# Kernel tuning notes

Hardware: AMD Instinct MI355X
Metric: run time of the kernel (lower is better)

## Reference

```python
import jax, jax.numpy as jnp
import numpy as np

HEAD_SIZE = 64
N_EMBD = 1024
BLOCK_SIZE = 2048


def setup_inputs() -> dict:
    key = jax.random.key(0)
    kx, kk, kq, kv = jax.random.split(key, 4)
    B, T = 8, 2048
    x = jax.random.normal(kx, (B, T, N_EMBD), dtype=jnp.float32)
    # nnx.Linear kernels have shape (in_features, out_features); lecun-normal-ish scale
    s = 1.0 / np.sqrt(N_EMBD)
    Wk = jax.random.normal(kk, (N_EMBD, HEAD_SIZE), dtype=jnp.float32) * s
    Wq = jax.random.normal(kq, (N_EMBD, HEAD_SIZE), dtype=jnp.float32) * s
    Wv = jax.random.normal(kv, (N_EMBD, HEAD_SIZE), dtype=jnp.float32) * s
    return {"x": x, "Wk": Wk, "Wq": Wq, "Wv": Wv}


def reference(x, Wk, Wq, Wv):
    B, T, C = x.shape
    k = jnp.einsum("btc,ch->bth", x, Wk)  # [B,T,H]
    q = jnp.einsum("btc,ch->bth", x, Wq)
    v = jnp.einsum("btc,ch->bth", x, Wv)
    # NOTE: original scales by C**-0.5 where C = n_embd (not head_size)
    scale = jnp.float32(C) ** -0.5
    wei = jnp.einsum("bth,bsh->bts", q, k) * scale  # [B,T,T]
    causal = jnp.tril(jnp.ones((T, T), dtype=bool))
    wei = jnp.where(causal, wei, -jnp.inf)
    wei = jax.nn.softmax(wei, axis=-1)
    # dropout_rate = 0.0 -> identity
    out = jnp.einsum("bts,bsh->bth", wei, v)  # [B,T,H]
    return out
```

## Files before the change

### kernel.cpp

```cpp
#include <hip/hip_runtime.h>
#include <hip/hip_bf16.h>

#define TT 2048
#define BATCH 8
#define MROWS (BATCH*TT)
#define AW 8

typedef __attribute__((ext_vector_type(8))) short bf16x8;
typedef __attribute__((ext_vector_type(4))) short s16x4;
typedef __attribute__((ext_vector_type(4))) float f32x4;

__device__ __forceinline__ short f2bf(float f) {
    union { __hip_bfloat16 h; short s; } u;
    u.h = __float2bfloat16(f);
    return u.s;
}
__device__ __forceinline__ float bf2f(short s) {
    union { unsigned u; float f; } u;
    u.u = ((unsigned)(unsigned short)s) << 16;
    return u.f;
}

typedef __attribute__((address_space(3))) unsigned int       lds_u32_t;
typedef const __attribute__((address_space(1))) unsigned int g_u32_t;
__device__ __forceinline__ void gl_lds16(const void* g, void* l) {
    __builtin_amdgcn_global_load_lds((g_u32_t*)g, (lds_u32_t*)l, 16, 0, 0);
}

__global__ __launch_bounds__(256) void wtrans_kernel(
    const float* __restrict__ Wk, const float* __restrict__ Wq,
    const float* __restrict__ Wv, short* __restrict__ wt)
{
    __shared__ float tile[64][68];
    const int mat = blockIdx.x >> 4;
    const int k0  = (blockIdx.x & 15) * 64;
    const float* W = (mat == 0) ? Wq : (mat == 1) ? Wk : Wv;
    const float scl = (mat == 0) ? 0.04508422002778011f : 1.0f;
    const int t = threadIdx.x;
    const int row = t >> 2, quad = t & 3;
    #pragma unroll
    for (int i = 0; i < 4; i++) {
        float4 v = *(const float4*)(W + (size_t)(k0 + row) * 64 + quad * 16 + i * 4);
        *(float4*)&tile[row][quad * 16 + i * 4] = v;
    }
    __syncthreads();
    short tmp[16];
    #pragma unroll
    for (int j = 0; j < 16; j++) tmp[j] = f2bf(tile[quad * 16 + j][row] * scl);
    short* dst = wt + (size_t)(mat * 64 + row) * 1024 + k0 + quad * 16;
    #pragma unroll
    for (int j2 = 0; j2 < 2; j2++) {
        bf16x8 o;
        #pragma unroll
        for (int jj = 0; jj < 8; jj++) o[jj] = tmp[j2 * 8 + jj];
        *(bf16x8*)(dst + j2 * 8) = o;
    }
}

__global__ __launch_bounds__(512, 2) void proj_kernel(
    const float* __restrict__ x, const short* __restrict__ wt,
    short* __restrict__ qb, short* __restrict__ kb, short* __restrict__ vtb)
{
    __shared__ __align__(16) char lds[131072];

    const int tid  = threadIdx.x;
    const int lane = tid & 63, w = tid >> 6;
    const int l15  = lane & 15, g = lane >> 4;
    const int x7   = l15 & 7;
    const int wr   = w & 1;
    const int wc   = w >> 1;
    const int r0   = blockIdx.x * 64;

    const int arow_s = tid >> 3, aseg = tid & 7;
    const float* xsrc = x + (size_t)(r0 + arow_s) * 1024 + aseg * 16;
    const int ac0 = ((aseg * 2)     ^ (arow_s & 7)) * 16;
    const int ac1 = ((aseg * 2 + 1) ^ (arow_s & 7)) * 16;
    char* const arow_lds0 = lds + arow_s * 256;

    const short* bg[6]; unsigned bOff[6];
    #pragma unroll
    for (int j = 0; j < 6; j++) {
        const int jp   = w * 6 + j;
        const int row  = jp * 4 + (lane >> 4);
        const int slot = (lane & 15) ^ (row & 7);
        bg[j]   = wt + (size_t)row * 1024 + slot * 8;
        bOff[j] = 32768 + jp * 1024;
    }

    f32x4 acc[2][3];
    #pragma unroll
    for (int rt = 0; rt < 2; rt++)
        #pragma unroll
        for (int nt = 0; nt < 3; nt++) acc[rt][nt] = (f32x4){0.f, 0.f, 0.f, 0.f};

    {
        float4 a0 = *(const float4*)(xsrc);
        float4 a1 = *(const float4*)(xsrc + 4);
        float4 a2 = *(const float4*)(xsrc + 8);
        float4 a3 = *(const float4*)(xsrc + 12);
        #pragma unroll
        for (int j = 0; j < 6; j++) gl_lds16(bg[j], lds + bOff[j]);
        bf16x8 c0 = { f2bf(a0.x), f2bf(a0.y), f2bf(a0.z), f2bf(a0.w),
                      f2bf(a1.x), f2bf(a1.y), f2bf(a1.z), f2bf(a1.w) };
        bf16x8 c1 = { f2bf(a2.x), f2bf(a2.y), f2bf(a2.z), f2bf(a2.w),
                      f2bf(a3.x), f2bf(a3.y), f2bf(a3.z), f2bf(a3.w) };
        *(bf16x8*)(arow_lds0 + ac0) = c0;
        *(bf16x8*)(arow_lds0 + ac1) = c1;
    }
    __syncthreads();

    #pragma unroll
    for (int ks = 0; ks < 8; ks++) {
        const int cur = ks & 1;
        const int nb  = cur ^ 1;

        float4 a0, a1, a2, a3;
        if (ks < 7) {
            a0 = *(const float4*)(xsrc + (ks + 1) * 128);
            a1 = *(const float4*)(xsrc + (ks + 1) * 128 + 4);
            a2 = *(const float4*)(xsrc + (ks + 1) * 128 + 8);
            a3 = *(const float4*)(xsrc + (ks + 1) * 128 + 12);
            #pragma unroll
            for (int j = 0; j < 6; j++)
                gl_lds16(bg[j] + (ks + 1) * 128, lds + nb * 49152 + bOff[j]);
        }

        const char*  Ab = lds + cur * 16384;
        const short* Bb = (const short*)(lds + 32768 + cur * 49152);

        bf16x8 af[2][4];
        #pragma unroll
        for (int rt = 0; rt < 2; rt++) {
            const int arow = wr * 32 + rt * 16 + l15;
            #pragma unroll
            for (int kc = 0; kc < 4; kc++)
                af[rt][kc] = *(const bf16x8*)(
                    Ab + arow * 256 + (((kc * 4 + g) ^ x7) * 16));
        }
        bf16x8 bfr[3][4];
        #pragma unroll
        for (int nt = 0; nt < 3; nt++)
            #pragma unroll
            for (int kc = 0; kc < 4; kc++)
                bfr[nt][kc] = *(const bf16x8*)(
                    Bb + (wc * 48 + nt * 16 + l15) * 128 + (((kc * 4 + g) ^ x7) * 8));

        #pragma unroll
        for (int kc = 0; kc < 4; kc++)
            #pragma unroll
            for (int rt = 0; rt < 2; rt++)
                #pragma unroll
                for (int nt = 0; nt < 3; nt++)
                    acc[rt][nt] = __builtin_amdgcn_mfma_f32_16x16x32_bf16(
                        af[rt][kc], bfr[nt][kc], acc[rt][nt], 0, 0, 0);

        if (ks < 7) {
            bf16x8 c0 = { f2bf(a0.x), f2bf(a0.y), f2bf(a0.z), f2bf(a0.w),
                          f2bf(a1.x), f2bf(a1.y), f2bf(a1.z), f2bf(a1.w) };
            bf16x8 c1 = { f2bf(a2.x), f2bf(a2.y), f2bf(a2.z), f2bf(a2.w),
                          f2bf(a3.x), f2bf(a3.y), f2bf(a3.z), f2bf(a3.w) };
            *(bf16x8*)(lds + nb * 16384 + arow_s * 256 + ac0) = c0;
            *(bf16x8*)(lds + nb * 16384 + arow_s * 256 + ac1) = c1;
        }
        __syncthreads();
    }

    const int bi  = r0 >> 11;
    const int sl0 = r0 & 2047;
    short* vsl = (short*)lds;
    #pragma unroll
    for (int rt = 0; rt < 2; rt++)
        #pragma unroll
        for (int nt = 0; nt < 3; nt++) {
            const int c = wc * 48 + nt * 16 + l15;
            #pragma unroll
            for (int r = 0; r < 4; r++) {
                const int lrow = wr * 32 + rt * 16 + g * 4 + r;
                const short v = f2bf(acc[rt][nt][r]);
                if (c < 64)        qb[(size_t)(r0 + lrow) * 64 + c] = v;
                else if (c < 128)  kb[(size_t)(r0 + lrow) * 64 + (c - 64)] = v;
                else               vsl[lrow * 66 + (c - 128)] = v;
            }
        }
    __syncthreads();
    {
        const int col = tid >> 3, seg = tid & 7;
        short tmp[8];
        #pragma unroll
        for (int j = 0; j < 8; j++) tmp[j] = vsl[(seg * 8 + j) * 66 + col];
        bf16x8 o;
        #pragma unroll
        for (int jj = 0; jj < 8; jj++) o[jj] = tmp[jj];
        *(bf16x8*)(vtb + ((size_t)bi * 64 + col) * TT + sl0 + seg * 8) = o;
    }
}

__global__ __launch_bounds__(512, 2)
void attn_kernel(
    const short* __restrict__ qb, const short* __restrict__ kb,
    const short* __restrict__ vtb, float* __restrict__ out)
{
    __shared__ __align__(16) char smem[AW * 4608];
    __shared__ float ml[AW][64];

    const int tid  = threadIdx.x;
    const int w    = tid >> 6, lane = tid & 63;
    const int l15  = lane & 15, g = lane >> 4;
    const int b    = blockIdx.x & 7;
    const int qt   = 63 - (blockIdx.x >> 3);
    const int r0   = qt * 32;
    const int nkv  = (r0 >> 6) + 1;

    short* ps = (short*)(smem + w * 4608);

    const short* q  = qb  + (size_t)b * TT * 64;
    const short* k  = kb  + (size_t)b * TT * 64;
    const short* vt = vtb + (size_t)b * 64 * TT;

    bf16x8 qf[2][2];
    #pragma unroll
    for (int rt = 0; rt < 2; rt++)
        #pragma unroll
        for (int kc = 0; kc < 2; kc++)
            qf[rt][kc] = *(const bf16x8*)(q + (size_t)(r0 + rt * 16 + l15) * 64 + kc * 32 + g * 8);

    f32x4 o[2][4];
    float m_[2] = { -INFINITY, -INFINITY };
    float l_[2] = { 0.f, 0.f };
    #pragma unroll
    for (int rt = 0; rt < 2; rt++)
        #pragma unroll
        for (int ht = 0; ht < 4; ht++) o[rt][ht] = (f32x4){0.f, 0.f, 0.f, 0.f};

    bf16x8 kf[4][2];
    if (w < nkv) {
        #pragma unroll
        for (int nt = 0; nt < 4; nt++)
            #pragma unroll
            for (int kc = 0; kc < 2; kc++)
                kf[nt][kc] = *(const bf16x8*)(
                    k + (size_t)(w * 64 + nt * 16 + l15) * 64 + kc * 32 + g * 8);
    }

    for (int t = w; t < nkv; t += AW) {
        const int s0 = t * 64;
        const bool diag = (t == nkv - 1);
        const bool more = (t + AW < nkv);

        f32x4 s[2][4];
        #pragma unroll
        for (int rt = 0; rt < 2; rt++)
            #pragma unroll
            for (int nt = 0; nt < 4; nt++) s[rt][nt] = (f32x4){0.f, 0.f, 0.f, 0.f};
        #pragma unroll
        for (int kc = 0; kc < 2; kc++)
            #pragma unroll
            for (int rt = 0; rt < 2; rt++)
                #pragma unroll
                for (int nt = 0; nt < 4; nt++)
                    s[rt][nt] = __builtin_amdgcn_mfma_f32_16x16x32_bf16(
                        kf[nt][kc], qf[rt][kc], s[rt][nt], 0, 0, 0);

        bf16x8 vf[4][2];
        #pragma unroll
        for (int ht = 0; ht < 4; ht++)
            #pragma unroll
            for (int kc = 0; kc < 2; kc++)
                vf[ht][kc] = *(const bf16x8*)(
                    vt + (size_t)(ht * 16 + l15) * TT + s0 + kc * 32 + g * 8);
        bf16x8 kfn[4][2];
        if (more) {
            #pragma unroll
            for (int nt = 0; nt < 4; nt++)
                #pragma unroll
                for (int kc = 0; kc < 2; kc++)
                    kfn[nt][kc] = *(const bf16x8*)(
                        k + (size_t)(s0 + AW * 64 + nt * 16 + l15) * 64 + kc * 32 + g * 8);
        }

        if (diag) {
            #pragma unroll
            for (int rt = 0; rt < 2; rt++) {
                const int qg = r0 + rt * 16 + l15;
                #pragma unroll
                for (int nt = 0; nt < 4; nt++)
                    #pragma unroll
                    for (int r = 0; r < 4; r++)
                        if (s0 + nt * 16 + g * 4 + r > qg) s[rt][nt][r] = -INFINITY;
            }
        }

        #pragma unroll
        for (int rt = 0; rt < 2; rt++) {
            float a0 = fmaxf(fmaxf(s[rt][0][0], s[rt][0][1]), fmaxf(s[rt][0][2], s[rt][0][3]));
            float a1 = fmaxf(fmaxf(s[rt][1][0], s[rt][1][1]), fmaxf(s[rt][1][2], s[rt][1][3]));
            float a2 = fmaxf(fmaxf(s[rt][2][0], s[rt][2][1]), fmaxf(s[rt][2][2], s[rt][2][3]));
            float a3 = fmaxf(fmaxf(s[rt][3][0], s[rt][3][1]), fmaxf(s[rt][3][2], s[rt][3][3]));
            float tm = fmaxf(fmaxf(a0, a1), fmaxf(a2, a3));
            tm = fmaxf(tm, __shfl_xor(tm, 16));
            tm = fmaxf(tm, __shfl_xor(tm, 32));

            const float mn = fmaxf(m_[rt], tm);
            const float al = __builtin_amdgcn_exp2f(m_[rt] - mn);
            m_[rt] = mn;

            #pragma unroll
            for (int nt = 0; nt < 4; nt++)
                #pragma unroll
                for (int r = 0; r < 4; r++)
                    s[rt][nt][r] = __builtin_amdgcn_exp2f(s[rt][nt][r] - mn);

            float b0 = (s[rt][0][0] + s[rt][0][1]) + (s[rt][0][2] + s[rt][0][3]);
            float b1 = (s[rt][1][0] + s[rt][1][1]) + (s[rt][1][2] + s[rt][1][3]);
            float b2 = (s[rt][2][0] + s[rt][2][1]) + (s[rt][2][2] + s[rt][2][3]);
            float b3 = (s[rt][3][0] + s[rt][3][1]) + (s[rt][3][2] + s[rt][3][3]);
            float ts = (b0 + b1) + (b2 + b3);
            ts += __shfl_xor(ts, 16);
            ts += __shfl_xor(ts, 32);
            l_[rt] = l_[rt] * al + ts;

            float ab[4];
            #pragma unroll
            for (int r = 0; r < 4; r++) ab[r] = __shfl(al, g * 4 + r);
            #pragma unroll
            for (int ht = 0; ht < 4; ht++)
                #pragma unroll
                for (int r = 0; r < 4; r++)
                    o[rt][ht][r] *= ab[r];

            #pragma unroll
            for (int nt = 0; nt < 4; nt++) {
                s16x4 pk = { f2bf(s[rt][nt][0]), f2bf(s[rt][nt][1]),
                             f2bf(s[rt][nt][2]), f2bf(s[rt][nt][3]) };
                *(s16x4*)&ps[(rt * 16 + l15) * 72 + nt * 16 + g * 4] = pk;
            }
        }

        bf16x8 pf[2][2];
        #pragma unroll
        for (int rt = 0; rt < 2; rt++)
            #pragma unroll
            for (int kc = 0; kc < 2; kc++)
                pf[rt][kc] = *(const bf16x8*)&ps[(rt * 16 + l15) * 72 + kc * 32 + g * 8];
        #pragma unroll
        for (int kc = 0; kc < 2; kc++)
            #pragma unroll
            for (int rt = 0; rt < 2; rt++)
                #pragma unroll
                for (int ht = 0; ht < 4; ht++)
                    o[rt][ht] = __builtin_amdgcn_mfma_f32_16x16x32_bf16(
                        pf[rt][kc], vf[ht][kc], o[rt][ht], 0, 0, 0);

        if (more) {
            #pragma unroll
            for (int nt = 0; nt < 4; nt++)
                #pragma unroll
                for (int kc = 0; kc < 2; kc++)
                    kf[nt][kc] = kfn[nt][kc];
        }
    }

    if (g == 0) {
        #pragma unroll
        for (int rt = 0; rt < 2; rt++) {
            ml[w][rt * 16 + l15]      = m_[rt];
            ml[w][32 + rt * 16 + l15] = l_[rt];
        }
    }
    short* pO = ps;
    #pragma unroll
    for (int rt = 0; rt < 2; rt++)
        #pragma unroll
        for (int ht = 0; ht < 4; ht++)
            #pragma unroll
            for (int r = 0; r < 4; r++)
                pO[(rt * 16 + g * 4 + r) * 68 + ht * 16 + l15] = f2bf(o[rt][ht][r]);
    __syncthreads();

    {
        const int row = tid >> 4, seg = tid & 15;
        float gm = -INFINITY;
        #pragma unroll
        for (int w2 = 0; w2 < AW; w2++) gm = fmaxf(gm, ml[w2][row]);
        float accL = 0.f;
        float accO[4] = {0.f, 0.f, 0.f, 0.f};
        #pragma unroll
        for (int w2 = 0; w2 < AW; w2++) {
            const float sc = __builtin_amdgcn_exp2f(ml[w2][row] - gm);
            accL = fmaf(sc, ml[w2][32 + row], accL);
            const s16x4 ov = *(const s16x4*)((const short*)(smem + w2 * 4608) + row * 68 + seg * 4);
            #pragma unroll
            for (int j = 0; j < 4; j++)
                accO[j] = fmaf(sc, bf2f(ov[j]), accO[j]);
        }
        const float inv = 1.f / accL;
        float4 res = make_float4(accO[0] * inv, accO[1] * inv, accO[2] * inv, accO[3] * inv);
        *(float4*)(out + ((size_t)b * TT + r0 + row) * 64 + seg * 4) = res;
    }
}

extern "C" void kernel_launch(void* const* d_in, const int* in_sizes, int n_in,
                              void* d_out, int out_size, void* d_ws, size_t ws_size,
                              hipStream_t stream) {
    const float* x  = (const float*)d_in[0];
    const float* Wk = (const float*)d_in[1];
    const float* Wq = (const float*)d_in[2];
    const float* Wv = (const float*)d_in[3];
    float* outp = (float*)d_out;

    short* wt  = (short*)d_ws;
    short* qb  = wt + (size_t)192 * 1024;
    short* kb  = qb + (size_t)MROWS * 64;
    short* vtb = kb + (size_t)MROWS * 64;

    wtrans_kernel<<<48, 256, 0, stream>>>(Wk, Wq, Wv, wt);
    proj_kernel<<<MROWS / 64, 512, 0, stream>>>(x, wt, qb, kb, vtb);
    attn_kernel<<<BATCH * 64, 512, 0, stream>>>(qb, kb, vtb, outp);
}
```

Baseline: 51.17 us.

## Split projection GEMM into 32-row, half-width output tiles across four times more blocks

The Q/K/V projection kernel now gives each block 32 rows and half of the 192 output columns, selected by the low bit of the block index. Blocks shrink to 256 threads and 64 KB of LDS, and the grid grows fourfold. The aim is more resident blocks per CU and better load balance across CUs in what is likely a memory-bound stage. In exchange, every x row is loaded and converted to bf16 by two blocks, doubling x traffic unless caches absorb the repeat, and only the upper-half block writes the transposed V tile.

```diff
diff --git a/kernel.cpp b/kernel.cpp
--- a/kernel.cpp
+++ b/kernel.cpp
@@ -57,11 +57,11 @@
     }
 }
 
-__global__ __launch_bounds__(512, 2) void proj_kernel(
+__global__ __launch_bounds__(256, 2) void proj_kernel(
     const float* __restrict__ x, const short* __restrict__ wt,
     short* __restrict__ qb, short* __restrict__ kb, short* __restrict__ vtb)
 {
-    __shared__ __align__(16) char lds[131072];
+    __shared__ __align__(16) char lds[65536];
 
     const int tid  = threadIdx.x;
     const int lane = tid & 63, w = tid >> 6;
@@ -69,13 +69,13 @@
     const int x7   = l15 & 7;
     const int wr   = w & 1;
     const int wc   = w >> 1;
-    const int r0   = blockIdx.x * 64;
+    const int nh   = blockIdx.x & 1;
+    const int r0   = (blockIdx.x >> 1) * 32;
 
     const int arow_s = tid >> 3, aseg = tid & 7;
     const float* xsrc = x + (size_t)(r0 + arow_s) * 1024 + aseg * 16;
     const int ac0 = ((aseg * 2)     ^ (arow_s & 7)) * 16;
     const int ac1 = ((aseg * 2 + 1) ^ (arow_s & 7)) * 16;
-    char* const arow_lds0 = lds + arow_s * 256;
 
     const short* bg[6]; unsigned bOff[6];
     #pragma unroll
@@ -83,15 +83,13 @@
         const int jp   = w * 6 + j;
         const int row  = jp * 4 + (lane >> 4);
         const int slot = (lane & 15) ^ (row & 7);
-        bg[j]   = wt + (size_t)row * 1024 + slot * 8;
-        bOff[j] = 32768 + jp * 1024;
-    }
-
-    f32x4 acc[2][3];
-    #pragma unroll
-    for (int rt = 0; rt < 2; rt++)
-        #pragma unroll
-        for (int nt = 0; nt < 3; nt++) acc[rt][nt] = (f32x4){0.f, 0.f, 0.f, 0.f};
+        bg[j]   = wt + (size_t)(nh * 96 + row) * 1024 + slot * 8;
+        bOff[j] = jp * 1024;
+    }
+
+    f32x4 acc[3];
+    #pragma unroll
+    for (int nt = 0; nt < 3; nt++) acc[nt] = (f32x4){0.f, 0.f, 0.f, 0.f};
 
     {
         float4 a0 = *(const float4*)(xsrc);
@@ -99,13 +97,13 @@
         float4 a2 = *(const float4*)(xsrc + 8);
         float4 a3 = *(const float4*)(xsrc + 12);
         #pragma unroll
-        for (int j = 0; j < 6; j++) gl_lds16(bg[j], lds + bOff[j]);
+        for (int j = 0; j < 6; j++) gl_lds16(bg[j], lds + 16384 + bOff[j]);
         bf16x8 c0 = { f2bf(a0.x), f2bf(a0.y), f2bf(a0.z), f2bf(a0.w),
                       f2bf(a1.x), f2bf(a1.y), f2bf(a1.z), f2bf(a1.w) };
         bf16x8 c1 = { f2bf(a2.x), f2bf(a2.y), f2bf(a2.z), f2bf(a2.w),
                       f2bf(a3.x), f2bf(a3.y), f2bf(a3.z), f2bf(a3.w) };
-        *(bf16x8*)(arow_lds0 + ac0) = c0;
-        *(bf16x8*)(arow_lds0 + ac1) = c1;
+        *(bf16x8*)(lds + arow_s * 256 + ac0) = c0;
+        *(bf16x8*)(lds + arow_s * 256 + ac1) = c1;
     }
     __syncthreads();
 
@@ -122,20 +120,18 @@
             a3 = *(const float4*)(xsrc + (ks + 1) * 128 + 12);
             #pragma unroll
             for (int j = 0; j < 6; j++)
-                gl_lds16(bg[j] + (ks + 1) * 128, lds + nb * 49152 + bOff[j]);
-        }
-
-        const char*  Ab = lds + cur * 16384;
-        const short* Bb = (const short*)(lds + 32768 + cur * 49152);
-
-        bf16x8 af[2][4];
-        #pragma unroll
-        for (int rt = 0; rt < 2; rt++) {
-            const int arow = wr * 32 + rt * 16 + l15;
+                gl_lds16(bg[j] + (ks + 1) * 128, lds + 16384 + nb * 24576 + bOff[j]);
+        }
+
+        const char*  Ab = lds + cur * 8192;
+        const short* Bb = (const short*)(lds + 16384 + cur * 24576);
+
+        bf16x8 af[4];
+        {
+            const int arow = wr * 16 + l15;
             #pragma unroll
             for (int kc = 0; kc < 4; kc++)
-                af[rt][kc] = *(const bf16x8*)(
-                    Ab + arow * 256 + (((kc * 4 + g) ^ x7) * 16));
+                af[kc] = *(const bf16x8*)(Ab + arow * 256 + (((kc * 4 + g) ^ x7) * 16));
         }
         bf16x8 bfr[3][4];
         #pragma unroll
@@ -148,19 +144,17 @@
         #pragma unroll
         for (int kc = 0; kc < 4; kc++)
             #pragma unroll
-            for (int rt = 0; rt < 2; rt++)
-                #pragma unroll
-                for (int nt = 0; nt < 3; nt++)
-                    acc[rt][nt] = __builtin_amdgcn_mfma_f32_16x16x32_bf16(
-                        af[rt][kc], bfr[nt][kc], acc[rt][nt], 0, 0, 0);
+            for (int nt = 0; nt < 3; nt++)
+                acc[nt] = __builtin_amdgcn_mfma_f32_16x16x32_bf16(
+                    af[kc], bfr[nt][kc], acc[nt], 0, 0, 0);
 
         if (ks < 7) {
             bf16x8 c0 = { f2bf(a0.x), f2bf(a0.y), f2bf(a0.z), f2bf(a0.w),
                           f2bf(a1.x), f2bf(a1.y), f2bf(a1.z), f2bf(a1.w) };
             bf16x8 c1 = { f2bf(a2.x), f2bf(a2.y), f2bf(a2.z), f2bf(a2.w),
                           f2bf(a3.x), f2bf(a3.y), f2bf(a3.z), f2bf(a3.w) };
-            *(bf16x8*)(lds + nb * 16384 + arow_s * 256 + ac0) = c0;
-            *(bf16x8*)(lds + nb * 16384 + arow_s * 256 + ac1) = c1;
+            *(bf16x8*)(lds + nb * 8192 + arow_s * 256 + ac0) = c0;
+            *(bf16x8*)(lds + nb * 8192 + arow_s * 256 + ac1) = c1;
         }
         __syncthreads();
     }
@@ -169,22 +163,21 @@
     const int sl0 = r0 & 2047;
     short* vsl = (short*)lds;
     #pragma unroll
-    for (int rt = 0; rt < 2; rt++)
-        #pragma unroll
-        for (int nt = 0; nt < 3; nt++) {
-            const int c = wc * 48 + nt * 16 + l15;
-            #pragma unroll
-            for (int r = 0; r < 4; r++) {
-                const int lrow = wr * 32 + rt * 16 + g * 4 + r;
-                const short v = f2bf(acc[rt][nt][r]);
-                if (c < 64)        qb[(size_t)(r0 + lrow) * 64 + c] = v;
-                else if (c < 128)  kb[(size_t)(r0 + lrow) * 64 + (c - 64)] = v;
-                else               vsl[lrow * 66 + (c - 128)] = v;
-            }
-        }
+    for (int nt = 0; nt < 3; nt++) {
+        const int c = nh * 96 + wc * 48 + nt * 16 + l15;
+        #pragma unroll
+        for (int r = 0; r < 4; r++) {
+            const int lrow = wr * 16 + g * 4 + r;
+            const int row  = r0 + lrow;
+            const short v = f2bf(acc[nt][r]);
+            if (c < 64)        qb[(size_t)row * 64 + c] = v;
+            else if (c < 128)  kb[(size_t)row * 64 + (c - 64)] = v;
+            else               vsl[lrow * 66 + (c - 128)] = v;
+        }
+    }
     __syncthreads();
-    {
-        const int col = tid >> 3, seg = tid & 7;
+    if (nh == 1) {
+        const int col = tid >> 2, seg = tid & 3;
         short tmp[8];
         #pragma unroll
         for (int j = 0; j < 8; j++) tmp[j] = vsl[(seg * 8 + j) * 66 + col];
@@ -414,6 +407,6 @@
     short* vtb = kb + (size_t)MROWS * 64;
 
     wtrans_kernel<<<48, 256, 0, stream>>>(Wk, Wq, Wv, wt);
-    proj_kernel<<<MROWS / 64, 512, 0, stream>>>(x, wt, qb, kb, vtb);
+    proj_kernel<<<(MROWS / 32) * 2, 256, 0, stream>>>(x, wt, qb, kb, vtb);
     attn_kernel<<<BATCH * 64, 512, 0, stream>>>(qb, kb, vtb, outp);
 }
```

Measured after the change: 69.47 us. 1.36x slower.
